# Performance work log

Measured on AMD Instinct MI355X. Metric: run time of the kernel, lower is better.

Reference implementation:

```python
import jax, jax.numpy as jnp
import numpy as np


def setup_inputs() -> dict:
    key = jax.random.key(0)
    k1, k2, k3 = jax.random.split(key, 3)
    backbone_feature = jax.random.normal(k1, (8, 256), dtype=jnp.float32)
    grouping_result = jax.random.randint(k2, (8,), 0, 32, dtype=jnp.int64)
    feature = jax.random.normal(k3, (8, 32, 48, 48, 48), dtype=jnp.float32)
    return {"backbone_feature": backbone_feature,
            "grouping_result": grouping_result,
            "feature": feature}


def reference(backbone_feature, grouping_result, feature):
    # feature: [B, R, W, H, D]
    B, R, W, H, D = feature.shape
    dt = feature.dtype
    mgr = feature.mean()  # global mean over all samples/regions/voxels

    # --- per-region argmax position (first occurrence, matching strict '>' scan) ---
    flat = feature.reshape(B, R, W * H * D)
    am = jnp.argmax(flat, axis=-1)                      # [B, R]
    max_x = (am // (H * D)).astype(dt)                  # [B, R]
    max_y = ((am // D) % H).astype(dt)
    max_z = (am % D).astype(dt)

    i = jnp.arange(W, dtype=dt).reshape(1, 1, W, 1, 1)
    j = jnp.arange(H, dtype=dt).reshape(1, 1, 1, H, 1)
    k = jnp.arange(D, dtype=dt).reshape(1, 1, 1, 1, D)

    dx2 = (max_x[:, :, None, None, None] - i) ** 2      # [B,R,W,1,1]
    dy2 = (max_y[:, :, None, None, None] - j) ** 2      # [B,R,1,H,1]
    dz2 = (max_z[:, :, None, None, None] - k) ** 2      # [B,R,1,1,D]

    f2 = feature * feature
    # NOTE: faithful to original parenthesization: z-term is NOT weighted by region^2
    dis_loss = jnp.sum(f2 * (dx2 + dy2)) + jnp.sum(jnp.broadcast_to(dz2, (B, R, W, H, D)))

    # --- exclude-self max over regions via top-2 along region axis ---
    srt = jnp.sort(feature, axis=1)                     # ascending along R
    m1 = srt[:, -1]                                     # [B, W, H, D] max over regions
    m2 = srt[:, -2]                                     # second max
    argmax_r = jnp.argmax(feature, axis=1)              # [B, W, H, D] first-occurrence
    r_ids = jnp.arange(R).reshape(1, R, 1, 1, 1)
    max_others = jnp.where(r_ids == argmax_r[:, None], m2[:, None], m1[:, None])  # [B,R,W,H,D]

    div_loss = jnp.sum(f2 * (max_others - mgr) ** 2)

    sum_num = B * R * W * H * D
    return (jnp.reshape(dis_loss / sum_num, (1,)),
            jnp.reshape(div_loss / sum_num, (1,)))
```

## Files before the change

kernel.cpp:

```cpp
#include <hip/hip_runtime.h>
#include <math.h>

#define W48 48
#define HD 2304
#define WHD 110592
#define NR 32
#define NB 8
#define QPP 27648
#define CHUNKS 108
#define MAIN_BLOCKS 864
#define NTOT 28311552.0

struct PPart { float s0, sx, sy; unsigned key; unsigned idx; };

__global__ __launch_bounds__(256, 2)
void k_main(const float* __restrict__ feat, PPart* __restrict__ pp,
            double* __restrict__ blk) {
  __shared__ float    lds_s0[16 * 256];
  __shared__ unsigned lds_key[16 * 256];
  __shared__ unsigned lds_mc[256];
  __shared__ float comb_s0[256], comb_sx[256], comb_sy[256];
  __shared__ unsigned comb_key[256], comb_idx[256];
  __shared__ double ld[4][5];

  const int bid = blockIdx.x;
  const int t = threadIdx.x;
  const int b = bid / CHUNKS;
  const int chunk = bid - b * CHUNKS;
  const int qbase = chunk * 256 + t;
  const float4* gptr = reinterpret_cast<const float4*>(feat) + (size_t)b * (NR * QPP) + qbase;

  const int p0 = qbase * 4;
  const float fi = (float)(p0 / HD);
  const float fj = (float)((p0 / W48) % W48);
  const float rrq = fi * fi + fj * fj;

  float v1[4], v2[4], cp[4];
#pragma unroll
  for (int c = 0; c < 4; ++c) { v1[c] = -INFINITY; v2[c] = -INFINITY; cp[c] = 0.f; }
  float ssum = 0.f, sii = 0.f;
  unsigned mcpack = 0u;

  float4 nb0 = gptr[0];
  float4 nb1 = gptr[(size_t)QPP];
  float4 nb2 = gptr[2 * (size_t)QPP];
  float4 nb3 = gptr[3 * (size_t)QPP];
  float4 nb4 = gptr[4 * (size_t)QPP];
  float4 nb5 = gptr[5 * (size_t)QPP];

  for (int half = 0; half < 2; ++half) {
#pragma unroll 4
    for (int rr = 0; rr < 16; ++rr) {
      const int r = half * 16 + rr;
      float4 v = nb0;
      nb0 = nb1; nb1 = nb2; nb2 = nb3; nb3 = nb4; nb4 = nb5;
      int rn = r + 6; rn = (rn < NR) ? rn : (NR - 1);
      nb5 = gptr[(size_t)rn * QPP];

      float vv[4] = {v.x, v.y, v.z, v.w};
      float f2[4];
#pragma unroll
      for (int c = 0; c < 4; ++c) {
        float f = vv[c];
        f2[c] = f * f;
        cp[c] += f2[c];
        ssum += f;
        float nv2 = fmaxf(f, v2[c]);
        v2[c] = (f > v1[c]) ? v1[c] : nv2;
        v1[c] = fmaxf(v1[c], f);
      }
      float s0t = (f2[0] + f2[1]) + (f2[2] + f2[3]);
      sii += s0t * rrq;

      float mv = vv[0]; int mc = 0;
#pragma unroll
      for (int c = 1; c < 4; ++c) { if (vv[c] > mv) { mv = vv[c]; mc = c; } }
      unsigned u = __float_as_uint(mv);
      unsigned key = u ^ ((unsigned)((int)u >> 31) | 0x80000000u);

      mcpack |= (unsigned)mc << (2 * rr);
      lds_s0[rr * 256 + t] = s0t;
      lds_key[rr * 256 + t] = key;
    }

    lds_mc[t] = mcpack; mcpack = 0u;
    __syncthreads();
    const int er = t & 15;
    const int eg = t >> 4;
    float es0 = 0.f, esx = 0.f, esy = 0.f;
    unsigned bk = 0u; int brow = 0;
#pragma unroll
    for (int k = 0; k < 16; ++k) {
      int row = eg * 16 + ((k + er) & 15);
      float s0v   = lds_s0[er * 256 + row];
      unsigned kv = lds_key[er * 256 + row];
      unsigned q = (unsigned)(chunk * 256 + row);
      float fiq = (float)(q / 576u);
      float fjq = (float)((q / 12u) % 48u);
      es0 += s0v;
      esx = fmaf(s0v, fiq, esx);
      esy = fmaf(s0v, fjq, esy);
      if (kv > bk || (kv == bk && row < brow)) { bk = kv; brow = row; }
    }
    unsigned wmc = (lds_mc[brow] >> (2 * er)) & 3u;
    unsigned bidx = (unsigned)((chunk * 256 + brow) * 4) + wmc;
    __syncthreads();
    comb_s0[t] = es0; comb_sx[t] = esx; comb_sy[t] = esy;
    comb_key[t] = bk; comb_idx[t] = bidx;
    __syncthreads();
    if (t < 16) {
      float ps0 = 0.f, psx = 0.f, psy = 0.f;
      unsigned fk = 0u, fidx = 0xffffffffu;
#pragma unroll
      for (int g2 = 0; g2 < 16; ++g2) {
        int ii = g2 * 16 + t;
        ps0 += comb_s0[ii]; psx += comb_sx[ii]; psy += comb_sy[ii];
        unsigned ck = comb_key[ii], ci = comb_idx[ii];
        if (ck > fk || (ck == fk && ci < fidx)) { fk = ck; fidx = ci; }
      }
      int plane = b * NR + half * 16 + t;
      PPart o; o.s0 = ps0; o.sx = psx; o.sy = psy; o.key = fk; o.idx = fidx;
      pp[(size_t)plane * CHUNKS + chunk] = o;
    }
    __syncthreads();
  }

  float A = 0.f, Bs = 0.f, C = 0.f;
#pragma unroll
  for (int c = 0; c < 4; ++c) {
    float m1 = v1[c], m1sq = m1 * m1;
    float rest = cp[c] - m1sq;
    A  += m1sq * rest + v2[c] * v2[c] * m1sq;
    Bs += m1 * rest + v2[c] * m1sq;
    C  += cp[c];
  }
  double dA = A, dB = Bs, dC = C, dS = ssum, dI = sii;
  const int wave = t >> 6, lane = t & 63;
#pragma unroll
  for (int off = 32; off; off >>= 1) {
    dA += __shfl_down(dA, off);
    dB += __shfl_down(dB, off);
    dC += __shfl_down(dC, off);
    dS += __shfl_down(dS, off);
    dI += __shfl_down(dI, off);
  }
  if (lane == 0) { ld[wave][0]=dA; ld[wave][1]=dB; ld[wave][2]=dC; ld[wave][3]=dS; ld[wave][4]=dI; }
  __syncthreads();
  if (t == 0) {
    double a=0, bb=0, cc=0, ss=0, si=0;
#pragma unroll
    for (int w = 0; w < 4; ++w) { a+=ld[w][0]; bb+=ld[w][1]; cc+=ld[w][2]; ss+=ld[w][3]; si+=ld[w][4]; }
    blk[(size_t)bid*5+0]=a; blk[(size_t)bid*5+1]=bb; blk[(size_t)bid*5+2]=cc;
    blk[(size_t)bid*5+3]=ss; blk[(size_t)bid*5+4]=si;
  }
}

__global__ __launch_bounds__(128)
void k_planes(const PPart* __restrict__ pp, double* __restrict__ planeDis) {
  const int p = blockIdx.x;
  const int t = threadIdx.x;
  double s0 = 0, sx = 0, sy = 0;
  unsigned fkey = 0, idx = 0xffffffffu;
  if (t < CHUNKS) {
    PPart v = pp[(size_t)p * CHUNKS + t];
    s0 = v.s0; sx = v.sx; sy = v.sy; fkey = v.key; idx = v.idx;
  }
#pragma unroll
  for (int off = 32; off; off >>= 1) {
    s0 += __shfl_down(s0, off);
    sx += __shfl_down(sx, off);
    sy += __shfl_down(sy, off);
    unsigned ok = __shfl_down(fkey, off);
    unsigned oi = __shfl_down(idx, off);
    if (ok > fkey || (ok == fkey && oi < idx)) { fkey = ok; idx = oi; }
  }
  __shared__ double ls[2][3];
  __shared__ unsigned lk[2][2];
  const int wave = t >> 6, lane = t & 63;
  if (lane == 0) { ls[wave][0]=s0; ls[wave][1]=sx; ls[wave][2]=sy; lk[wave][0]=fkey; lk[wave][1]=idx; }
  __syncthreads();
  if (t == 0) {
    double a0=0, a1=0, a2=0; unsigned bk=0, bi=0xffffffffu;
#pragma unroll
    for (int w = 0; w < 2; ++w) {
      a0 += ls[w][0]; a1 += ls[w][1]; a2 += ls[w][2];
      if (lk[w][0] > bk || (lk[w][0]==bk && lk[w][1] < bi)) { bk = lk[w][0]; bi = lk[w][1]; }
    }
    int am = (int)bi;
    int mx = am / HD;
    int rem = am - mx * HD;
    int my = rem / W48;
    int mz = rem - my * W48;
    double dmx = mx, dmy = my, dmz = mz;
    planeDis[p] = (dmx*dmx + dmy*dmy) * a0 - 2.0*dmx*a1 - 2.0*dmy*a2
                + 2304.0 * (48.0*dmz*dmz - 2256.0*dmz + 35720.0);
  }
}

__global__ __launch_bounds__(256)
void k_fin(const double* __restrict__ planeDis, const double* __restrict__ blk,
           float* __restrict__ out) {
  const int t = threadIdx.x;
  double dis = planeDis[t];
  double A = 0, B = 0, C = 0, S = 0, SII = 0;
  for (int i = t; i < MAIN_BLOCKS; i += 256) {
    A   += blk[(size_t)i*5+0];
    B   += blk[(size_t)i*5+1];
    C   += blk[(size_t)i*5+2];
    S   += blk[(size_t)i*5+3];
    SII += blk[(size_t)i*5+4];
  }
#pragma unroll
  for (int off = 32; off; off >>= 1) {
    dis += __shfl_down(dis, off);
    A   += __shfl_down(A, off);
    B   += __shfl_down(B, off);
    C   += __shfl_down(C, off);
    S   += __shfl_down(S, off);
    SII += __shfl_down(SII, off);
  }
  __shared__ double ls[4][6];
  const int wave = t >> 6, lane = t & 63;
  if (lane == 0) {
    ls[wave][0]=dis; ls[wave][1]=A; ls[wave][2]=B; ls[wave][3]=C; ls[wave][4]=S; ls[wave][5]=SII;
  }
  __syncthreads();
  if (t == 0) {
    double td=0, tA=0, tB=0, tC=0, tS=0, tI=0;
#pragma unroll
    for (int w = 0; w < 4; ++w) {
      td+=ls[w][0]; tA+=ls[w][1]; tB+=ls[w][2]; tC+=ls[w][3]; tS+=ls[w][4]; tI+=ls[w][5];
    }
    double mgr = tS / NTOT;
    out[0] = (float)((td + tI) / NTOT);
    out[1] = (float)((tA - 2.0*mgr*tB + mgr*mgr*tC) / NTOT);
  }
}

extern "C" void kernel_launch(void* const* d_in, const int* in_sizes, int n_in,
                              void* d_out, int out_size, void* d_ws, size_t ws_size,
                              hipStream_t stream) {
  const float* feat = (const float*)d_in[2];
  float* out = (float*)d_out;

  PPart* pp = (PPart*)d_ws;
  double* blk = (double*)((char*)d_ws + 552960);
  double* planeDis = (double*)((char*)d_ws + 552960 + 34560);

  k_main<<<MAIN_BLOCKS, 256, 0, stream>>>(feat, pp, blk);
  k_planes<<<256, 128, 0, stream>>>(pp, planeDis);
  k_fin<<<1, 256, 0, stream>>>(planeDis, blk, out);
}
```

Measured before the change: 39.66 us.

## Use per-wave partial reductions and fuse plane and final kernels via atomic counter

The main kernel now reduces each 16-plane half inside each wave using per-wave LDS slices and xor shuffles. This removes the block-wide __syncthreads barriers and the combine stage, at the cost of writing four times as many per-plane partials. The plane-reduction and final-reduction kernels are merged into one tail kernel, where the last block (found with an atomic counter) computes the outputs. This drops one kernel launch but adds a memset before the kernels and a threadfence plus atomic per block.

```diff
diff --git a/kernel.cpp b/kernel.cpp
--- a/kernel.cpp
+++ b/kernel.cpp
@@ -3,32 +3,40 @@
 
 #define W48 48
 #define HD 2304
-#define WHD 110592
 #define NR 32
-#define NB 8
 #define QPP 27648
 #define CHUNKS 108
 #define MAIN_BLOCKS 864
+#define PARTS 432
+#define NPLANES 256
 #define NTOT 28311552.0
 
 struct PPart { float s0, sx, sy; unsigned key; unsigned idx; };
+
+#define PP_BYTES 2211840u
+#define BLK_OFF  2211840u
+#define PD_OFF   2246400u
+#define CNT_OFF  2248448u
 
 __global__ __launch_bounds__(256, 2)
 void k_main(const float* __restrict__ feat, PPart* __restrict__ pp,
             double* __restrict__ blk) {
-  __shared__ float    lds_s0[16 * 256];
-  __shared__ unsigned lds_key[16 * 256];
-  __shared__ unsigned lds_mc[256];
-  __shared__ float comb_s0[256], comb_sx[256], comb_sy[256];
-  __shared__ unsigned comb_key[256], comb_idx[256];
+  __shared__ float    lds_s0[4][16 * 64];
+  __shared__ unsigned lds_key[4][16 * 64];
+  __shared__ unsigned lds_mc[4][64];
   __shared__ double ld[4][5];
 
   const int bid = blockIdx.x;
   const int t = threadIdx.x;
+  const int wave = t >> 6, lane = t & 63;
   const int b = bid / CHUNKS;
   const int chunk = bid - b * CHUNKS;
   const int qbase = chunk * 256 + t;
   const float4* gptr = reinterpret_cast<const float4*>(feat) + (size_t)b * (NR * QPP) + qbase;
+
+  float* __restrict__ ws0 = lds_s0[wave];
+  unsigned* __restrict__ wkey = lds_key[wave];
+  unsigned* __restrict__ wmcA = lds_mc[wave];
 
   const int p0 = qbase * 4;
   const float fi = (float)(p0 / HD);
@@ -79,50 +87,50 @@
       unsigned key = u ^ ((unsigned)((int)u >> 31) | 0x80000000u);
 
       mcpack |= (unsigned)mc << (2 * rr);
-      lds_s0[rr * 256 + t] = s0t;
-      lds_key[rr * 256 + t] = key;
-    }
-
-    lds_mc[t] = mcpack; mcpack = 0u;
-    __syncthreads();
-    const int er = t & 15;
-    const int eg = t >> 4;
+      ws0[rr * 64 + lane] = s0t;
+      wkey[rr * 64 + lane] = key;
+    }
+
+    wmcA[lane] = mcpack; mcpack = 0u;
+    __asm__ __volatile__("" ::: "memory");
+    __builtin_amdgcn_wave_barrier();
+
+    const int er = lane & 15;
+    const int eg = lane >> 4;
     float es0 = 0.f, esx = 0.f, esy = 0.f;
     unsigned bk = 0u; int brow = 0;
 #pragma unroll
     for (int k = 0; k < 16; ++k) {
       int row = eg * 16 + ((k + er) & 15);
-      float s0v   = lds_s0[er * 256 + row];
-      unsigned kv = lds_key[er * 256 + row];
-      unsigned q = (unsigned)(chunk * 256 + row);
-      float fiq = (float)(q / 576u);
-      float fjq = (float)((q / 12u) % 48u);
+      float s0v   = ws0[er * 64 + row];
+      unsigned kv = wkey[er * 64 + row];
+      unsigned g = (unsigned)(chunk * 256 + wave * 64 + row);
+      float fiq = (float)(g / 576u);
+      float fjq = (float)((g / 12u) % 48u);
       es0 += s0v;
       esx = fmaf(s0v, fiq, esx);
       esy = fmaf(s0v, fjq, esy);
       if (kv > bk || (kv == bk && row < brow)) { bk = kv; brow = row; }
     }
-    unsigned wmc = (lds_mc[brow] >> (2 * er)) & 3u;
-    unsigned bidx = (unsigned)((chunk * 256 + brow) * 4) + wmc;
-    __syncthreads();
-    comb_s0[t] = es0; comb_sx[t] = esx; comb_sy[t] = esy;
-    comb_key[t] = bk; comb_idx[t] = bidx;
-    __syncthreads();
-    if (t < 16) {
-      float ps0 = 0.f, psx = 0.f, psy = 0.f;
-      unsigned fk = 0u, fidx = 0xffffffffu;
-#pragma unroll
-      for (int g2 = 0; g2 < 16; ++g2) {
-        int ii = g2 * 16 + t;
-        ps0 += comb_s0[ii]; psx += comb_sx[ii]; psy += comb_sy[ii];
-        unsigned ck = comb_key[ii], ci = comb_idx[ii];
-        if (ck > fk || (ck == fk && ci < fidx)) { fk = ck; fidx = ci; }
-      }
-      int plane = b * NR + half * 16 + t;
-      PPart o; o.s0 = ps0; o.sx = psx; o.sy = psy; o.key = fk; o.idx = fidx;
-      pp[(size_t)plane * CHUNKS + chunk] = o;
-    }
-    __syncthreads();
+    unsigned wmc = (wmcA[brow] >> (2 * er)) & 3u;
+    unsigned bidx = (unsigned)((chunk * 256 + wave * 64 + brow) * 4) + wmc;
+
+#pragma unroll
+    for (int m = 16; m <= 32; m <<= 1) {
+      es0 += __shfl_xor(es0, m);
+      esx += __shfl_xor(esx, m);
+      esy += __shfl_xor(esy, m);
+      unsigned ok = (unsigned)__shfl_xor((int)bk, m);
+      unsigned oi = (unsigned)__shfl_xor((int)bidx, m);
+      if (ok > bk || (ok == bk && oi < bidx)) { bk = ok; bidx = oi; }
+    }
+    if (lane < 16) {
+      int plane = b * NR + half * 16 + lane;
+      PPart o; o.s0 = es0; o.sx = esx; o.sy = esy; o.key = bk; o.idx = bidx;
+      pp[(size_t)plane * PARTS + chunk * 4 + wave] = o;
+    }
+    __builtin_amdgcn_wave_barrier();
+    __asm__ __volatile__("" ::: "memory");
   }
 
   float A = 0.f, Bs = 0.f, C = 0.f;
@@ -135,7 +143,6 @@
     C  += cp[c];
   }
   double dA = A, dB = Bs, dC = C, dS = ssum, dI = sii;
-  const int wave = t >> 6, lane = t & 63;
 #pragma unroll
   for (int off = 32; off; off >>= 1) {
     dA += __shfl_down(dA, off);
@@ -156,36 +163,44 @@
 }
 
 __global__ __launch_bounds__(128)
-void k_planes(const PPart* __restrict__ pp, double* __restrict__ planeDis) {
+void k_tail(const PPart* __restrict__ pp, const double* __restrict__ blk,
+            double* __restrict__ planeDis, unsigned* __restrict__ counter,
+            float* __restrict__ out) {
+  __shared__ double ls[2][3];
+  __shared__ unsigned lk[2][2];
+  __shared__ double fin[2][6];
+  __shared__ int lastFlag;
+
   const int p = blockIdx.x;
   const int t = threadIdx.x;
+  const int wave = t >> 6, lane = t & 63;
+
   double s0 = 0, sx = 0, sy = 0;
-  unsigned fkey = 0, idx = 0xffffffffu;
-  if (t < CHUNKS) {
-    PPart v = pp[(size_t)p * CHUNKS + t];
-    s0 = v.s0; sx = v.sx; sy = v.sy; fkey = v.key; idx = v.idx;
+  unsigned key = 0, idx = 0xffffffffu;
+#pragma unroll
+  for (int k = 0; k < 4; ++k) {
+    int i = t + 128 * k;
+    if (i < PARTS) {
+      PPart v = pp[(size_t)p * PARTS + i];
+      s0 += v.s0; sx += v.sx; sy += v.sy;
+      if (v.key > key || (v.key == key && v.idx < idx)) { key = v.key; idx = v.idx; }
+    }
   }
 #pragma unroll
   for (int off = 32; off; off >>= 1) {
     s0 += __shfl_down(s0, off);
     sx += __shfl_down(sx, off);
     sy += __shfl_down(sy, off);
-    unsigned ok = __shfl_down(fkey, off);
-    unsigned oi = __shfl_down(idx, off);
-    if (ok > fkey || (ok == fkey && oi < idx)) { fkey = ok; idx = oi; }
-  }
-  __shared__ double ls[2][3];
-  __shared__ unsigned lk[2][2];
-  const int wave = t >> 6, lane = t & 63;
-  if (lane == 0) { ls[wave][0]=s0; ls[wave][1]=sx; ls[wave][2]=sy; lk[wave][0]=fkey; lk[wave][1]=idx; }
+    unsigned ok = (unsigned)__shfl_down((int)key, off);
+    unsigned oi = (unsigned)__shfl_down((int)idx, off);
+    if (ok > key || (ok == key && oi < idx)) { key = ok; idx = oi; }
+  }
+  if (lane == 0) { ls[wave][0]=s0; ls[wave][1]=sx; ls[wave][2]=sy; lk[wave][0]=key; lk[wave][1]=idx; }
   __syncthreads();
   if (t == 0) {
-    double a0=0, a1=0, a2=0; unsigned bk=0, bi=0xffffffffu;
-#pragma unroll
-    for (int w = 0; w < 2; ++w) {
-      a0 += ls[w][0]; a1 += ls[w][1]; a2 += ls[w][2];
-      if (lk[w][0] > bk || (lk[w][0]==bk && lk[w][1] < bi)) { bk = lk[w][0]; bi = lk[w][1]; }
-    }
+    double a0 = ls[0][0] + ls[1][0], a1 = ls[0][1] + ls[1][1], a2 = ls[0][2] + ls[1][2];
+    unsigned bk = lk[0][0], bi = lk[0][1];
+    if (lk[1][0] > bk || (lk[1][0] == bk && lk[1][1] < bi)) { bk = lk[1][0]; bi = lk[1][1]; }
     int am = (int)bi;
     int mx = am / HD;
     int rem = am - mx * HD;
@@ -194,46 +209,44 @@
     double dmx = mx, dmy = my, dmz = mz;
     planeDis[p] = (dmx*dmx + dmy*dmy) * a0 - 2.0*dmx*a1 - 2.0*dmy*a2
                 + 2304.0 * (48.0*dmz*dmz - 2256.0*dmz + 35720.0);
-  }
-}
-
-__global__ __launch_bounds__(256)
-void k_fin(const double* __restrict__ planeDis, const double* __restrict__ blk,
-           float* __restrict__ out) {
-  const int t = threadIdx.x;
-  double dis = planeDis[t];
-  double A = 0, B = 0, C = 0, S = 0, SII = 0;
-  for (int i = t; i < MAIN_BLOCKS; i += 256) {
-    A   += blk[(size_t)i*5+0];
-    B   += blk[(size_t)i*5+1];
-    C   += blk[(size_t)i*5+2];
-    S   += blk[(size_t)i*5+3];
-    SII += blk[(size_t)i*5+4];
-  }
-#pragma unroll
-  for (int off = 32; off; off >>= 1) {
-    dis += __shfl_down(dis, off);
-    A   += __shfl_down(A, off);
-    B   += __shfl_down(B, off);
-    C   += __shfl_down(C, off);
-    S   += __shfl_down(S, off);
-    SII += __shfl_down(SII, off);
-  }
-  __shared__ double ls[4][6];
-  const int wave = t >> 6, lane = t & 63;
-  if (lane == 0) {
-    ls[wave][0]=dis; ls[wave][1]=A; ls[wave][2]=B; ls[wave][3]=C; ls[wave][4]=S; ls[wave][5]=SII;
+    __threadfence();
+    lastFlag = (atomicAdd(counter, 1u) == NPLANES - 1u);
   }
   __syncthreads();
-  if (t == 0) {
-    double td=0, tA=0, tB=0, tC=0, tS=0, tI=0;
-#pragma unroll
-    for (int w = 0; w < 4; ++w) {
-      td+=ls[w][0]; tA+=ls[w][1]; tB+=ls[w][2]; tC+=ls[w][3]; tS+=ls[w][4]; tI+=ls[w][5];
-    }
-    double mgr = tS / NTOT;
-    out[0] = (float)((td + tI) / NTOT);
-    out[1] = (float)((tA - 2.0*mgr*tB + mgr*mgr*tC) / NTOT);
+
+  if (lastFlag) {
+    __threadfence();
+    double dis = planeDis[t] + planeDis[t + 128];
+    double A = 0, B = 0, C = 0, S = 0, SI = 0;
+#pragma unroll
+    for (int k = 0; k < 7; ++k) {
+      int i = t + 128 * k;
+      if (i < MAIN_BLOCKS) {
+        const double* bb = blk + (size_t)i * 5;
+        A += bb[0]; B += bb[1]; C += bb[2]; S += bb[3]; SI += bb[4];
+      }
+    }
+#pragma unroll
+    for (int off = 32; off; off >>= 1) {
+      dis += __shfl_down(dis, off);
+      A   += __shfl_down(A, off);
+      B   += __shfl_down(B, off);
+      C   += __shfl_down(C, off);
+      S   += __shfl_down(S, off);
+      SI  += __shfl_down(SI, off);
+    }
+    if (lane == 0) {
+      fin[wave][0]=dis; fin[wave][1]=A; fin[wave][2]=B;
+      fin[wave][3]=C;   fin[wave][4]=S; fin[wave][5]=SI;
+    }
+    __syncthreads();
+    if (t == 0) {
+      double td = fin[0][0]+fin[1][0], tA = fin[0][1]+fin[1][1], tB = fin[0][2]+fin[1][2];
+      double tC = fin[0][3]+fin[1][3], tS = fin[0][4]+fin[1][4], tI = fin[0][5]+fin[1][5];
+      double mgr = tS / NTOT;
+      out[0] = (float)((td + tI) / NTOT);
+      out[1] = (float)((tA - 2.0*mgr*tB + mgr*mgr*tC) / NTOT);
+    }
   }
 }
 
@@ -243,11 +256,12 @@
   const float* feat = (const float*)d_in[2];
   float* out = (float*)d_out;
 
-  PPart* pp = (PPart*)d_ws;
-  double* blk = (double*)((char*)d_ws + 552960);
-  double* planeDis = (double*)((char*)d_ws + 552960 + 34560);
-
+  PPart* pp        = (PPart*)d_ws;
+  double* blk      = (double*)((char*)d_ws + BLK_OFF);
+  double* planeDis = (double*)((char*)d_ws + PD_OFF);
+  unsigned* cnt    = (unsigned*)((char*)d_ws + CNT_OFF);
+
+  hipMemsetAsync(cnt, 0, 4, stream);
   k_main<<<MAIN_BLOCKS, 256, 0, stream>>>(feat, pp, blk);
-  k_planes<<<256, 128, 0, stream>>>(pp, planeDis);
-  k_fin<<<1, 256, 0, stream>>>(planeDis, blk, out);
+  k_tail<<<NPLANES, 128, 0, stream>>>(pp, blk, planeDis, cnt, out);
 }
```

Result: slower. 47.48 us (+19.7%).
